# Kernel optimization log

Measured on AMD Instinct MI355X. Metric: run time of the kernel, lower is better.

Reference implementation:

```python
import jax, jax.numpy as jnp
import numpy as np
from jax.ops import segment_sum

N_NODES = 50000
N_EDGES = 800000
IN_DIM, HID_DIM, OUT_DIM = 128, 128, 64
N_GRAPHS = 64


def setup_inputs() -> dict:
    key = jax.random.key(0)
    ks = jax.random.split(key, 8)
    x = jax.random.normal(ks[0], (N_NODES, IN_DIM), dtype=jnp.float32)
    edge_index = jax.random.randint(ks[1], (2, N_EDGES), 0, N_NODES, dtype=jnp.int64)
    batch = jnp.sort(jax.random.randint(ks[2], (N_NODES,), 0, N_GRAPHS, dtype=jnp.int64))
    # Glorot-ish init for GCNConv linear weights, zero bias (PyG default)
    W1 = jax.random.normal(ks[3], (IN_DIM, HID_DIM), dtype=jnp.float32) / np.sqrt(IN_DIM)
    b1 = jnp.zeros((HID_DIM,), dtype=jnp.float32)
    W2 = jax.random.normal(ks[4], (HID_DIM, OUT_DIM), dtype=jnp.float32) / np.sqrt(HID_DIM)
    b2 = jnp.zeros((OUT_DIM,), dtype=jnp.float32)
    return {"x": x, "W1": W1, "b1": b1, "W2": W2, "b2": b2,
            "edge_index": edge_index, "batch": batch, "num_graphs": N_GRAPHS}


def _gcn_conv(h, W, b, src, dst, deg_inv_sqrt, n_nodes):
    # h: [N, Fin] -> [N, Fout]; GCNConv: D^{-1/2}(A+I)D^{-1/2} (h W) + b
    hw = h @ W                                   # [N, Fout]
    norm = deg_inv_sqrt[src] * deg_inv_sqrt[dst] # [E]
    msg = hw[src] * norm[:, None]                # [E, Fout] (gather)
    agg = segment_sum(msg, dst, num_segments=n_nodes)  # scatter-add
    # self-loop contribution: norm_ii = deg_inv_sqrt[i]^2
    agg = agg + hw * (deg_inv_sqrt * deg_inv_sqrt)[:, None]
    return agg + b


def reference(x, W1, b1, W2, b2, edge_index, batch, num_graphs):
    n_nodes = x.shape[0]
    src, dst = edge_index[0], edge_index[1]
    # degree of A + I (self-loops added, as in PyG GCNConv default)
    deg = segment_sum(jnp.ones_like(dst, dtype=x.dtype), dst,
                      num_segments=n_nodes) + 1.0
    deg_inv_sqrt = jax.lax.rsqrt(deg)

    h = jax.nn.relu(_gcn_conv(x, W1, b1, src, dst, deg_inv_sqrt, n_nodes))
    h = jax.nn.relu(_gcn_conv(h, W2, b2, src, dst, deg_inv_sqrt, n_nodes))

    # global_mean_pool over batch ids
    sums = segment_sum(h, batch, num_segments=num_graphs)          # [G, Fout]
    counts = segment_sum(jnp.ones((n_nodes,), dtype=h.dtype), batch,
                         num_segments=num_graphs)                  # [G]
    return sums / jnp.maximum(counts, 1.0)[:, None]
```

## Files before the change

kernel.cpp:

```cpp
#include <hip/hip_runtime.h>

typedef float f4 __attribute__((ext_vector_type(4)));
typedef float f2 __attribute__((ext_vector_type(2)));
typedef short s8 __attribute__((ext_vector_type(8)));

union FU { unsigned u[4]; s8 s; };

__device__ __forceinline__ unsigned cvtpk(float lo, float hi){
  unsigned r;
  asm("v_cvt_pk_bf16_f32 %0, %1, %2" : "=v"(r) : "v"(lo), "v"(hi));
  return r;
}

__device__ __forceinline__ float bflo(unsigned v){ return __uint_as_float(v << 16); }
__device__ __forceinline__ float bfhi(unsigned v){ return __uint_as_float(v & 0xFFFF0000u); }

__device__ __forceinline__ int ld_idx(const void* p, int i, int is64){
  if (is64) return (int)((const long long*)p)[i];
  return ((const int*)p)[i];
}

__device__ __forceinline__ int detect64(const unsigned* __restrict__ e_raw, int e){
  int lane = threadIdx.x & 63;
  int lim = (e < 1024) ? e : 1024;
  int nz = 0;
  for (int i = lane; i < lim; i += 64) nz |= (e_raw[2*i + 1] != 0u);
  return (__ballot(nz != 0) == 0ull) ? 1 : 0;
}

template<int NC, int BIN>
__device__ __forceinline__ void gemm_body(const void* __restrict__ Xv,
                                          const float* __restrict__ W,
                                          unsigned short* __restrict__ Yb,
                                          int n, int blk, char* Alds){
  constexpr int NCF = NC/16;
  constexpr int WPC = 8/NCF;
  constexpr int RT  = 8/WPC;
  const int tid  = threadIdx.x;
  const int wave = tid >> 6, lane = tid & 63;
  const int rb = blk * 128;

  const int cbase = (wave % NCF) * 16;
  const int rt0   = (wave / NCF) * RT;
  const int col   = cbase + (lane & 15);
  const int kr0   = (lane >> 4) * 8;
  FU bu[4];
#pragma unroll
  for (int ks = 0; ks < 4; ++ks){
    float wv[8];
#pragma unroll
    for (int j = 0; j < 8; ++j) wv[j] = W[(size_t)(ks*32 + kr0 + j)*NC + col];
#pragma unroll
    for (int q = 0; q < 4; ++q) bu[ks].u[q] = cvtpk(wv[2*q], wv[2*q+1]);
  }

  for (int i = tid; i < 128*32; i += 512){
    int row = i >> 5, kq = i & 31;
    int rsrc = rb + row; if (rsrc >= n) rsrc = n - 1;
    uint2 dw;
    if (BIN){
      dw = ((const uint2*)Xv)[(size_t)rsrc*32 + kq];
    } else {
      f4 xv = ((const f4*)Xv)[(size_t)rsrc*32 + kq];
      dw = make_uint2(cvtpk(xv[0], xv[1]), cvtpk(xv[2], xv[3]));
    }
    int byte = (row*256 + kq*8) ^ ((row & 7) << 4);
    *reinterpret_cast<uint2*>(Alds + byte) = dw;
  }
  __syncthreads();

  f4 acc[RT];
#pragma unroll
  for (int rt = 0; rt < RT; ++rt) acc[rt] = 0.0f;

#pragma unroll
  for (int rt = 0; rt < RT; ++rt){
    const int arow = (rt0 + rt)*16 + (lane & 15);
#pragma unroll
    for (int ks = 0; ks < 4; ++ks){
      int kb = ks*32 + kr0;
      int byte = (arow*256 + kb*2) ^ ((arow & 7) << 4);
      s8 a = *reinterpret_cast<const s8*>(Alds + byte);
      acc[rt] = __builtin_amdgcn_mfma_f32_16x16x32_bf16(a, bu[ks].s, acc[rt], 0, 0, 0);
    }
  }

#pragma unroll
  for (int rt = 0; rt < RT; ++rt){
    int rowb = rb + (rt0 + rt)*16 + 4*(lane >> 4);
#pragma unroll
    for (int r = 0; r < 4; ++r){
      int row = rowb + r;
      if (row < n) Yb[(size_t)row*NC + col] = (unsigned short)cvtpk(acc[rt][r], acc[rt][r]);
    }
  }
}

template<int NC, int BIN>
__global__ __launch_bounds__(512) void gemm_k(const void* __restrict__ X,
                                              const float* __restrict__ W,
                                              unsigned short* __restrict__ Yb, int n){
  __shared__ int4 AldsV[2048];
  gemm_body<NC, BIN>(X, W, Yb, n, blockIdx.x, (char*)AldsV);
}

__global__ __launch_bounds__(512) void fused1_k(const float* __restrict__ X,
                                                const float* __restrict__ W1,
                                                unsigned short* __restrict__ Yb,
                                                const void* __restrict__ eidx,
                                                const void* __restrict__ batchp,
                                                int* __restrict__ counts,
                                                unsigned* __restrict__ etmp,
                                                int* __restrict__ batch32,
                                                int n, int e, int GB, int CB){
  __shared__ int4 AldsV[2048];
  __shared__ int hist[512];
  int blk = blockIdx.x;
  if (blk < GB){
    gemm_body<128, 0>(X, W1, Yb, n, blk, (char*)AldsV);
    return;
  }
  blk -= GB;
  const int NBK = (n + 127) >> 7;
  for (int i = threadIdx.x; i < NBK; i += 512) hist[i] = 0;
  __syncthreads();
  int is64 = detect64((const unsigned*)eidx, e);
  int CHK = (e + CB - 1) / CB;
  int beg = blk*CHK, end = min(e, beg + CHK);
  for (int i = beg + (int)threadIdx.x; i < end; i += 512){
    int s = ld_idx(eidx, i, is64);
    int d = ld_idx(eidx, e + i, is64);
    atomicAdd(&hist[d >> 7], 1);
    etmp[i] = (unsigned)s | ((unsigned)(d & 127) << 16) | ((unsigned)(d >> 7) << 23);
  }
  __syncthreads();
  for (int i = threadIdx.x; i < NBK; i += 512) counts[i*CB + blk] = hist[i];
  for (int i = blk*512 + (int)threadIdx.x; i < n; i += CB*512)
    batch32[i] = ld_idx(batchp, i, is64);
}

__global__ void scanA_k(const int* __restrict__ counts, int* __restrict__ base,
                        int* __restrict__ bsum, int L,
                        const int* __restrict__ batch32, float* __restrict__ invc,
                        float* __restrict__ out, int n, int g){
  __shared__ int sh[256];
  __shared__ int starts[257];
  int tid = threadIdx.x;
  int i = blockIdx.x*256 + tid;
  int v = (i < L) ? counts[i] : 0;
  sh[tid] = v; __syncthreads();
  for (int off = 1; off < 256; off <<= 1){
    int t = (tid >= off) ? sh[tid - off] : 0;
    __syncthreads();
    sh[tid] += t;
    __syncthreads();
  }
  if (i < L) base[i] = sh[tid] - v;
  if (tid == 255) bsum[blockIdx.x] = sh[255];
  if (blockIdx.x == 0){
    if (tid <= g){
      int lo = 0, hi = n;
      while (lo < hi){ int mid = (lo + hi) >> 1; if (batch32[mid] < tid) lo = mid + 1; else hi = mid; }
      starts[tid] = lo;
    }
    __syncthreads();
    if (tid < g){
      float c = (float)(starts[tid + 1] - starts[tid]);
      invc[tid] = 1.0f / fmaxf(c, 1.0f);
    }
    for (int k = tid; k < (g << 6); k += 256) out[k] = 0.0f;
  }
}

__global__ __launch_bounds__(512) void scat_k(const unsigned* __restrict__ etmp,
                                              const int* __restrict__ base,
                                              const int* __restrict__ bsum,
                                              int* __restrict__ bsumS,
                                              int* __restrict__ packed,
                                              int n, int e, int CB){
  __shared__ int sh[512];
  __shared__ int cur[512];
  int blk = blockIdx.x, tid = threadIdx.x;
  const int NBK = (n + 127) >> 7;
  int v = (tid < NBK) ? bsum[tid] : 0;
  sh[tid] = v; __syncthreads();
  for (int o = 1; o < 512; o <<= 1){
    int t = (tid >= o) ? sh[tid - o] : 0;
    __syncthreads();
    sh[tid] += t;
    __syncthreads();
  }
  int ex = sh[tid] - v;
  if (tid < NBK) cur[tid] = ex + base[tid*CB + blk];
  if (blk == 0){
    if (tid < NBK) bsumS[tid] = ex;
    if (tid == NBK - 1) bsumS[NBK] = sh[tid];
  }
  __syncthreads();
  int CHK = (e + CB - 1) / CB;
  int beg = blk*CHK, end = min(e, beg + CHK);
  for (int i = beg + tid; i < end; i += 512){
    unsigned w = etmp[i];
    int pos = atomicAdd(&cur[w >> 23], 1);
    packed[pos] = (int)(w & 0x7FFFFFu);
  }
}

#define CSR_CAP 6144
__global__ __launch_bounds__(256) void csr_k(const int* __restrict__ packed,
                                             const int* __restrict__ bsumS,
                                             int* __restrict__ esrcS,
                                             int* __restrict__ rowptr,
                                             float* __restrict__ dinv, int n, int e){
  __shared__ int vals[CSR_CAP];
  __shared__ int hist[128], off[128], cur[128];
  int b = blockIdx.x, tid = threadIdx.x;
  if (b == 0 && tid == 0) rowptr[n] = e;
  int sbeg = bsumS[b], send = bsumS[b + 1];
  int m = send - sbeg;
  int mL = min(m, CSR_CAP);
  for (int i = tid; i < mL; i += 256) vals[i] = packed[sbeg + i];
  if (tid < 128) hist[tid] = 0;
  __syncthreads();
  for (int i = tid; i < m; i += 256){
    int v = (i < CSR_CAP) ? vals[i] : packed[sbeg + i];
    atomicAdd(&hist[(v >> 16) & 127], 1);
  }
  __syncthreads();
  if (tid < 128) off[tid] = hist[tid];
  __syncthreads();
  for (int o = 1; o < 128; o <<= 1){
    int v = 0;
    if (tid < 128 && tid >= o) v = off[tid - o];
    __syncthreads();
    if (tid < 128) off[tid] += v;
    __syncthreads();
  }
  if (tid < 128){
    int ex = off[tid] - hist[tid];
    cur[tid] = ex;
    int node = b*128 + tid;
    if (node < n){
      rowptr[node] = sbeg + ex;
      dinv[node] = rsqrtf((float)hist[tid] + 1.0f);
    }
  }
  __syncthreads();
  for (int i = tid; i < m; i += 256){
    int v = (i < CSR_CAP) ? vals[i] : packed[sbeg + i];
    int pos = atomicAdd(&cur[(v >> 16) & 127], 1);
    esrcS[sbeg + pos] = v & 0xFFFF;
  }
}

__global__ __launch_bounds__(256) void agg128_k(const unsigned short* __restrict__ HWb,
                                                const float* __restrict__ dinv,
                                                const int* __restrict__ rowptr,
                                                const int* __restrict__ esrcS,
                                                const float* __restrict__ bias,
                                                unsigned short* __restrict__ Hb, int n){
  int wid  = (blockIdx.x*256 + threadIdx.x) >> 6;
  int lane = threadIdx.x & 63;
  if (wid >= n) return;
  wid = __builtin_amdgcn_readfirstlane(wid);
  const int slot = lane >> 4;
  const int cg   = lane & 15;
  float di = dinv[wid];
  float di2 = di * di;
  int beg = __builtin_amdgcn_readfirstlane(rowptr[wid]);
  int end = __builtin_amdgcn_readfirstlane(rowptr[wid + 1]);
  float acc[8];
#pragma unroll
  for (int k = 0; k < 8; ++k) acc[k] = 0.0f;
  const char* Hc = (const char*)HWb;
  int j = beg;
  for (; j + 16 <= end; j += 16){
    int s[4]; float wt[4]; uint4 v[4];
#pragma unroll
    for (int q = 0; q < 4; ++q) s[q] = esrcS[j + q*4 + slot];
#pragma unroll
    for (int q = 0; q < 4; ++q){
      wt[q] = dinv[s[q]] * di;
      v[q] = *(const uint4*)(Hc + (size_t)s[q]*256 + cg*16);
    }
#pragma unroll
    for (int q = 0; q < 4; ++q){
      acc[0] += bflo(v[q].x)*wt[q]; acc[1] += bfhi(v[q].x)*wt[q];
      acc[2] += bflo(v[q].y)*wt[q]; acc[3] += bfhi(v[q].y)*wt[q];
      acc[4] += bflo(v[q].z)*wt[q]; acc[5] += bfhi(v[q].z)*wt[q];
      acc[6] += bflo(v[q].w)*wt[q]; acc[7] += bfhi(v[q].w)*wt[q];
    }
  }
  for (; j < end; j += 4){
    int idx = j + slot;
    int live = (idx < end);
    if (!live) idx = end - 1;
    int s = esrcS[idx];
    float wt = live ? (dinv[s] * di) : 0.0f;
    uint4 v = *(const uint4*)(Hc + (size_t)s*256 + cg*16);
    acc[0] += bflo(v.x)*wt; acc[1] += bfhi(v.x)*wt;
    acc[2] += bflo(v.y)*wt; acc[3] += bfhi(v.y)*wt;
    acc[4] += bflo(v.z)*wt; acc[5] += bfhi(v.z)*wt;
    acc[6] += bflo(v.w)*wt; acc[7] += bfhi(v.w)*wt;
  }
#pragma unroll
  for (int k = 0; k < 8; ++k){
    acc[k] += __shfl_xor(acc[k], 16);
    acc[k] += __shfl_xor(acc[k], 32);
  }
  uint4 sv = *(const uint4*)(Hc + (size_t)wid*256 + cg*16);
  acc[0] += bflo(sv.x)*di2; acc[1] += bfhi(sv.x)*di2;
  acc[2] += bflo(sv.y)*di2; acc[3] += bfhi(sv.y)*di2;
  acc[4] += bflo(sv.z)*di2; acc[5] += bfhi(sv.z)*di2;
  acc[6] += bflo(sv.w)*di2; acc[7] += bfhi(sv.w)*di2;
  f4 b0 = *(const f4*)(bias + cg*8);
  f4 b1 = *(const f4*)(bias + cg*8 + 4);
#pragma unroll
  for (int k = 0; k < 4; ++k) acc[k] = fmaxf(acc[k] + b0[k], 0.0f);
#pragma unroll
  for (int k = 0; k < 4; ++k) acc[4+k] = fmaxf(acc[4+k] + b1[k], 0.0f);
  if (slot == 0){
    uint4 o;
    o.x = cvtpk(acc[0], acc[1]); o.y = cvtpk(acc[2], acc[3]);
    o.z = cvtpk(acc[4], acc[5]); o.w = cvtpk(acc[6], acc[7]);
    *(uint4*)((char*)Hb + (size_t)wid*256 + cg*16) = o;
  }
}

__global__ __launch_bounds__(256) void agg64_k(const unsigned short* __restrict__ HWb,
                                               const float* __restrict__ dinv,
                                               const int* __restrict__ rowptr,
                                               const int* __restrict__ esrcS,
                                               const float* __restrict__ bias,
                                               float* __restrict__ H2, int n){
  int wid  = (blockIdx.x*256 + threadIdx.x) >> 6;
  int lane = threadIdx.x & 63;
  if (wid >= n) return;
  wid = __builtin_amdgcn_readfirstlane(wid);
  const int slot = lane >> 3;
  const int cg   = lane & 7;
  float di = dinv[wid];
  float di2 = di * di;
  int beg = __builtin_amdgcn_readfirstlane(rowptr[wid]);
  int end = __builtin_amdgcn_readfirstlane(rowptr[wid + 1]);
  float acc[8];
#pragma unroll
  for (int k = 0; k < 8; ++k) acc[k] = 0.0f;
  const char* Hc = (const char*)HWb;
  int j = beg;
  for (; j + 16 <= end; j += 16){
    int s[2]; float wt[2]; uint4 v[2];
#pragma unroll
    for (int q = 0; q < 2; ++q) s[q] = esrcS[j + q*8 + slot];
#pragma unroll
    for (int q = 0; q < 2; ++q){
      wt[q] = dinv[s[q]] * di;
      v[q] = *(const uint4*)(Hc + (size_t)s[q]*128 + cg*16);
    }
#pragma unroll
    for (int q = 0; q < 2; ++q){
      acc[0] += bflo(v[q].x)*wt[q]; acc[1] += bfhi(v[q].x)*wt[q];
      acc[2] += bflo(v[q].y)*wt[q]; acc[3] += bfhi(v[q].y)*wt[q];
      acc[4] += bflo(v[q].z)*wt[q]; acc[5] += bfhi(v[q].z)*wt[q];
      acc[6] += bflo(v[q].w)*wt[q]; acc[7] += bfhi(v[q].w)*wt[q];
    }
  }
  for (; j < end; j += 8){
    int idx = j + slot;
    int live = (idx < end);
    if (!live) idx = end - 1;
    int s = esrcS[idx];
    float wt = live ? (dinv[s] * di) : 0.0f;
    uint4 v = *(const uint4*)(Hc + (size_t)s*128 + cg*16);
    acc[0] += bflo(v.x)*wt; acc[1] += bfhi(v.x)*wt;
    acc[2] += bflo(v.y)*wt; acc[3] += bfhi(v.y)*wt;
    acc[4] += bflo(v.z)*wt; acc[5] += bfhi(v.z)*wt;
    acc[6] += bflo(v.w)*wt; acc[7] += bfhi(v.w)*wt;
  }
#pragma unroll
  for (int k = 0; k < 8; ++k){
    acc[k] += __shfl_xor(acc[k], 8);
    acc[k] += __shfl_xor(acc[k], 16);
    acc[k] += __shfl_xor(acc[k], 32);
  }
  uint4 sv = *(const uint4*)(Hc + (size_t)wid*128 + cg*16);
  acc[0] += bflo(sv.x)*di2; acc[1] += bfhi(sv.x)*di2;
  acc[2] += bflo(sv.y)*di2; acc[3] += bfhi(sv.y)*di2;
  acc[4] += bflo(sv.z)*di2; acc[5] += bfhi(sv.z)*di2;
  acc[6] += bflo(sv.w)*di2; acc[7] += bfhi(sv.w)*di2;
  f4 b0 = *(const f4*)(bias + cg*8);
  f4 b1 = *(const f4*)(bias + cg*8 + 4);
#pragma unroll
  for (int k = 0; k < 4; ++k) acc[k] = fmaxf(acc[k] + b0[k], 0.0f);
#pragma unroll
  for (int k = 0; k < 4; ++k) acc[4+k] = fmaxf(acc[4+k] + b1[k], 0.0f);
  if (slot == 0){
    f4 o0; o0[0]=acc[0]; o0[1]=acc[1]; o0[2]=acc[2]; o0[3]=acc[3];
    f4 o1; o1[0]=acc[4]; o1[1]=acc[5]; o1[2]=acc[6]; o1[3]=acc[7];
    *(f4*)(H2 + (size_t)wid*64 + cg*8)     = o0;
    *(f4*)(H2 + (size_t)wid*64 + cg*8 + 4) = o1;
  }
}

__global__ __launch_bounds__(256) void pool_k(const float* __restrict__ H2,
                                              const int* __restrict__ batch32,
                                              const float* __restrict__ invc,
                                              float* __restrict__ out, int n){
  int wid  = (blockIdx.x*256 + threadIdx.x) >> 6;
  int lane = threadIdx.x & 63;
  int start = wid * 8;
  if (start >= n) return;
  int cnt = min(8, n - start);
  float v[8]; int b[8];
#pragma unroll
  for (int t = 0; t < 8; ++t){
    int i = start + t; if (i >= n) i = n - 1;
    v[t] = H2[(size_t)i*64 + lane];
    b[t] = batch32[i];
  }
  float acc = 0.0f;
  int gcur = b[0];
#pragma unroll
  for (int t = 0; t < 8; ++t){
    if (t < cnt){
      if (b[t] != gcur){
        unsafeAtomicAdd(&out[gcur*64 + lane], acc * invc[gcur]);
        acc = 0.0f; gcur = b[t];
      }
      acc += v[t];
    }
  }
  unsafeAtomicAdd(&out[gcur*64 + lane], acc * invc[gcur]);
}

extern "C" void kernel_launch(void* const* d_in, const int* in_sizes, int n_in,
                              void* d_out, int out_size, void* d_ws, size_t ws_size,
                              hipStream_t stream){
  const float* x    = (const float*)d_in[0];
  const float* W1   = (const float*)d_in[1];
  const float* b1   = (const float*)d_in[2];
  const float* W2   = (const float*)d_in[3];
  const float* b2   = (const float*)d_in[4];
  const void*  eidx = d_in[5];
  const void*  batchp = d_in[6];
  const int n = in_sizes[0] / 128;
  const int e = in_sizes[5] / 2;
  const int g = out_size / 64;
  float* out = (float*)d_out;

  const int NBK = (n + 127) >> 7;
  const int CB  = 256;
  const int GB  = (n + 127) / 128;
  const int L   = NBK * CB;

  char* w = (char*)d_ws;
  int* counts  = (int*)w;
  int* base    = counts + (size_t)L;
  int* bsum    = base + (size_t)L;
  int* bsumS   = bsum + NBK;
  int* rowptr  = bsumS + (NBK + 1);
  int* batch32 = rowptr + (n + 1);
  float* dinv  = (float*)(batch32 + n);
  float* invc  = dinv + n;
  unsigned* etmp = (unsigned*)(invc + g);
  int* packed  = (int*)(etmp + e);
  int* esrcS   = packed + e;
  size_t ofs = (size_t)((char*)(esrcS + e) - w);
  ofs = (ofs + 255) & ~(size_t)255;
  unsigned short* HWb = (unsigned short*)(w + ofs);
  size_t ofs2 = ofs + (size_t)n * 128 * 2;
  ofs2 = (ofs2 + 255) & ~(size_t)255;
  unsigned short* Hb = (unsigned short*)(w + ofs2);
  size_t ofs3 = ofs2 + (size_t)n * 128 * 2;
  ofs3 = (ofs3 + 255) & ~(size_t)255;
  float* H2 = (float*)(w + ofs3);

  fused1_k<<<GB + CB, 512, 0, stream>>>(x, W1, HWb, eidx, batchp,
                                        counts, etmp, batch32, n, e, GB, CB);
  scanA_k<<<NBK, 256, 0, stream>>>(counts, base, bsum, L, batch32, invc, out, n, g);
  scat_k<<<CB, 512, 0, stream>>>(etmp, base, bsum, bsumS, packed, n, e, CB);
  csr_k<<<NBK, 256, 0, stream>>>(packed, bsumS, esrcS, rowptr, dinv, n, e);

  agg128_k<<<(n + 3)/4, 256, 0, stream>>>(HWb, dinv, rowptr, esrcS, b1, Hb, n);
  gemm_k<64, 1><<<GB, 512, 0, stream>>>(Hb, W2, HWb, n);
  agg64_k<<<(n + 3)/4, 256, 0, stream>>>(HWb, dinv, rowptr, esrcS, b2, H2, n);

  int pw = (n + 7)/8;
  pool_k<<<(pw + 3)/4, 256, 0, stream>>>(H2, batch32, invc, out, n);
}
```

Before: 116.2 us.

## Fuse second-layer weight multiply into first aggregation kernel epilogue

The first-layer aggregation kernel now multiplies each aggregated hidden row by W2 in its epilogue, using a bf16 transposed copy of W2 staged in shared memory, and writes the 64-wide HW2 directly. This removes the separate GEMM launch and the round trip of the 128-wide hidden activations through global memory. In exchange, every 4-node block reloads and converts the full W2 into LDS. The per-node product is a scalar 64-term dot per lane instead of MFMA, which adds ALU and LDS work to an otherwise memory-bound gather kernel.

```diff
diff --git a/kernel.cpp b/kernel.cpp
--- a/kernel.cpp
+++ b/kernel.cpp
@@ -28,20 +28,16 @@
   return (__ballot(nz != 0) == 0ull) ? 1 : 0;
 }
 
-template<int NC, int BIN>
-__device__ __forceinline__ void gemm_body(const void* __restrict__ Xv,
-                                          const float* __restrict__ W,
-                                          unsigned short* __restrict__ Yb,
-                                          int n, int blk, char* Alds){
-  constexpr int NCF = NC/16;
-  constexpr int WPC = 8/NCF;
-  constexpr int RT  = 8/WPC;
+__device__ __forceinline__ void gemm_body128(const float* __restrict__ Xv,
+                                             const float* __restrict__ W,
+                                             unsigned short* __restrict__ Yb,
+                                             int n, int blk, char* Alds){
+  constexpr int NC = 128;
   const int tid  = threadIdx.x;
   const int wave = tid >> 6, lane = tid & 63;
   const int rb = blk * 128;
 
-  const int cbase = (wave % NCF) * 16;
-  const int rt0   = (wave / NCF) * RT;
+  const int cbase = wave * 16;
   const int col   = cbase + (lane & 15);
   const int kr0   = (lane >> 4) * 8;
   FU bu[4];
@@ -57,25 +53,20 @@
   for (int i = tid; i < 128*32; i += 512){
     int row = i >> 5, kq = i & 31;
     int rsrc = rb + row; if (rsrc >= n) rsrc = n - 1;
-    uint2 dw;
-    if (BIN){
-      dw = ((const uint2*)Xv)[(size_t)rsrc*32 + kq];
-    } else {
-      f4 xv = ((const f4*)Xv)[(size_t)rsrc*32 + kq];
-      dw = make_uint2(cvtpk(xv[0], xv[1]), cvtpk(xv[2], xv[3]));
-    }
+    f4 xv = ((const f4*)Xv)[(size_t)rsrc*32 + kq];
+    uint2 dw = make_uint2(cvtpk(xv[0], xv[1]), cvtpk(xv[2], xv[3]));
     int byte = (row*256 + kq*8) ^ ((row & 7) << 4);
     *reinterpret_cast<uint2*>(Alds + byte) = dw;
   }
   __syncthreads();
 
-  f4 acc[RT];
-#pragma unroll
-  for (int rt = 0; rt < RT; ++rt) acc[rt] = 0.0f;
-
-#pragma unroll
-  for (int rt = 0; rt < RT; ++rt){
-    const int arow = (rt0 + rt)*16 + (lane & 15);
+  f4 acc[8];
+#pragma unroll
+  for (int rt = 0; rt < 8; ++rt) acc[rt] = 0.0f;
+
+#pragma unroll
+  for (int rt = 0; rt < 8; ++rt){
+    const int arow = rt*16 + (lane & 15);
 #pragma unroll
     for (int ks = 0; ks < 4; ++ks){
       int kb = ks*32 + kr0;
@@ -86,22 +77,14 @@
   }
 
 #pragma unroll
-  for (int rt = 0; rt < RT; ++rt){
-    int rowb = rb + (rt0 + rt)*16 + 4*(lane >> 4);
+  for (int rt = 0; rt < 8; ++rt){
+    int rowb = rb + rt*16 + 4*(lane >> 4);
 #pragma unroll
     for (int r = 0; r < 4; ++r){
       int row = rowb + r;
       if (row < n) Yb[(size_t)row*NC + col] = (unsigned short)cvtpk(acc[rt][r], acc[rt][r]);
     }
   }
-}
-
-template<int NC, int BIN>
-__global__ __launch_bounds__(512) void gemm_k(const void* __restrict__ X,
-                                              const float* __restrict__ W,
-                                              unsigned short* __restrict__ Yb, int n){
-  __shared__ int4 AldsV[2048];
-  gemm_body<NC, BIN>(X, W, Yb, n, blockIdx.x, (char*)AldsV);
 }
 
 __global__ __launch_bounds__(512) void fused1_k(const float* __restrict__ X,
@@ -117,7 +100,7 @@
   __shared__ int hist[512];
   int blk = blockIdx.x;
   if (blk < GB){
-    gemm_body<128, 0>(X, W1, Yb, n, blk, (char*)AldsV);
+    gemm_body128(X, W1, Yb, n, blk, (char*)AldsV);
     return;
   }
   blk -= GB;
@@ -253,15 +236,28 @@
   }
 }
 
-__global__ __launch_bounds__(256) void agg128_k(const unsigned short* __restrict__ HWb,
-                                                const float* __restrict__ dinv,
-                                                const int* __restrict__ rowptr,
-                                                const int* __restrict__ esrcS,
-                                                const float* __restrict__ bias,
-                                                unsigned short* __restrict__ Hb, int n){
-  int wid  = (blockIdx.x*256 + threadIdx.x) >> 6;
-  int lane = threadIdx.x & 63;
-  if (wid >= n) return;
+__global__ __launch_bounds__(256) void agg128mv_k(const unsigned short* __restrict__ HWb,
+                                                  const float* __restrict__ dinv,
+                                                  const int* __restrict__ rowptr,
+                                                  const int* __restrict__ esrcS,
+                                                  const float* __restrict__ bias,
+                                                  const float* __restrict__ W2,
+                                                  unsigned short* __restrict__ HW2b,
+                                                  int n){
+  __shared__ unsigned W2t[64*65];
+  __shared__ unsigned h1buf[4*64];
+  const int tid = threadIdx.x;
+  for (int idx = tid; idx < 64*64; idx += 256){
+    int c = idx & 63, kk = idx >> 6;
+    W2t[c*65 + kk] = cvtpk(W2[(size_t)(2*kk)*64 + c], W2[(size_t)(2*kk+1)*64 + c]);
+  }
+  __syncthreads();
+
+  int wid  = (blockIdx.x*256 + tid) >> 6;
+  const int lane = tid & 63;
+  const int wave = tid >> 6;
+  const bool valid = (wid < n);
+  if (wid >= n) wid = n - 1;
   wid = __builtin_amdgcn_readfirstlane(wid);
   const int slot = lane >> 4;
   const int cg   = lane & 15;
@@ -319,12 +315,23 @@
   for (int k = 0; k < 4; ++k) acc[k] = fmaxf(acc[k] + b0[k], 0.0f);
 #pragma unroll
   for (int k = 0; k < 4; ++k) acc[4+k] = fmaxf(acc[4+k] + b1[k], 0.0f);
+
   if (slot == 0){
-    uint4 o;
-    o.x = cvtpk(acc[0], acc[1]); o.y = cvtpk(acc[2], acc[3]);
-    o.z = cvtpk(acc[4], acc[5]); o.w = cvtpk(acc[6], acc[7]);
-    *(uint4*)((char*)Hb + (size_t)wid*256 + cg*16) = o;
-  }
+#pragma unroll
+    for (int q = 0; q < 4; ++q)
+      h1buf[wave*64 + cg*4 + q] = cvtpk(acc[2*q], acc[2*q+1]);
+  }
+  asm volatile("s_waitcnt lgkmcnt(0)" ::: "memory");
+
+  const int c = lane;
+  float o = 0.0f;
+#pragma unroll 16
+  for (int kk = 0; kk < 64; ++kk){
+    unsigned hp = h1buf[wave*64 + kk];
+    unsigned wv = W2t[c*65 + kk];
+    o += bflo(hp)*bflo(wv) + bfhi(hp)*bfhi(wv);
+  }
+  if (valid) HW2b[(size_t)wid*64 + c] = (unsigned short)cvtpk(o, o);
 }
 
 __global__ __launch_bounds__(256) void agg64_k(const unsigned short* __restrict__ HWb,
@@ -470,8 +477,8 @@
   unsigned short* HWb = (unsigned short*)(w + ofs);
   size_t ofs2 = ofs + (size_t)n * 128 * 2;
   ofs2 = (ofs2 + 255) & ~(size_t)255;
-  unsigned short* Hb = (unsigned short*)(w + ofs2);
-  size_t ofs3 = ofs2 + (size_t)n * 128 * 2;
+  unsigned short* HW2b = (unsigned short*)(w + ofs2);
+  size_t ofs3 = ofs2 + (size_t)n * 64 * 2;
   ofs3 = (ofs3 + 255) & ~(size_t)255;
   float* H2 = (float*)(w + ofs3);
 
@@ -481,9 +488,9 @@
   scat_k<<<CB, 512, 0, stream>>>(etmp, base, bsum, bsumS, packed, n, e, CB);
   csr_k<<<NBK, 256, 0, stream>>>(packed, bsumS, esrcS, rowptr, dinv, n, e);
 
-  agg128_k<<<(n + 3)/4, 256, 0, stream>>>(HWb, dinv, rowptr, esrcS, b1, Hb, n);
-  gemm_k<64, 1><<<GB, 512, 0, stream>>>(Hb, W2, HWb, n);
-  agg64_k<<<(n + 3)/4, 256, 0, stream>>>(HWb, dinv, rowptr, esrcS, b2, H2, n);
+  agg128mv_k<<<(n + 3)/4, 256, 0, stream>>>(HWb, dinv, rowptr, esrcS, b1, W2,
+                                            HW2b, n);
+  agg64_k<<<(n + 3)/4, 256, 0, stream>>>(HW2b, dinv, rowptr, esrcS, b2, H2, n);
 
   int pw = (n + 7)/8;
   pool_k<<<(pw + 3)/4, 256, 0, stream>>>(H2, batch32, invc, out, n);
```

Result: slower. 159.2 us (+37.0%).
